# Kernel optimization log

Measured on AMD Instinct MI355X. Metric: run time of the kernel, lower is better.

Reference implementation:

```python
import jax, jax.numpy as jnp
import numpy as np

B_SZ, NX, IN_DIM = 32, 16384, 3
DIM, J, MODE, RANK, FC_DIM, OUT_DIM, N_LAYERS = 64, 16, 128, 4, 128, 1, 3


def setup_inputs() -> dict:
    key = jax.random.key(0)
    ks = jax.random.split(key, 20)
    scale = 1.0 / (MODE * MODE)
    s_out = 1.0 / MODE
    x = jax.random.normal(ks[0], (B_SZ, NX, IN_DIM), jnp.float32)
    bases = jax.random.normal(ks[1], (NX, MODE), jnp.float32) / np.sqrt(NX)
    wbases = jax.random.normal(ks[2], (NX, MODE), jnp.float32) / np.sqrt(NX)
    product = bases.T @ wbases  # (MODE_out, MODE_in)
    D_out = np.sqrt(s_out) * jax.random.uniform(ks[3], (J, MODE), jnp.float32)
    D_in = np.sqrt(s_out) * jax.random.uniform(ks[4], (J, MODE), jnp.float32)
    A = s_out * jax.random.uniform(ks[5], (J, RANK, MODE), jnp.float32)
    Bm = s_out * jax.random.uniform(ks[6], (J, RANK, MODE), jnp.float32)
    W_sp = scale * jax.random.normal(ks[7], (N_LAYERS, DIM, DIM, J), jnp.float32)
    W_conv = jax.random.normal(ks[8], (N_LAYERS, DIM, DIM), jnp.float32) / np.sqrt(DIM)
    b_conv = jnp.zeros((N_LAYERS, DIM), jnp.float32)
    W0 = jax.random.normal(ks[9], (IN_DIM, DIM), jnp.float32) / np.sqrt(IN_DIM)
    b0 = jnp.zeros((DIM,), jnp.float32)
    W1 = jax.random.normal(ks[10], (DIM, FC_DIM), jnp.float32) / np.sqrt(DIM)
    b1 = jnp.zeros((FC_DIM,), jnp.float32)
    W2 = jax.random.normal(ks[11], (FC_DIM, OUT_DIM), jnp.float32) / np.sqrt(FC_DIM)
    b2 = jnp.zeros((OUT_DIM,), jnp.float32)
    return {"x": x, "bases": bases, "wbases": wbases, "product": product,
            "D_out": D_out, "D_in": D_in, "A": A, "Bm": Bm,
            "W_sp": W_sp, "W_conv": W_conv, "b_conv": b_conv,
            "W0": W0, "b0": b0, "W1": W1, "b1": b1, "W2": W2, "b2": b2}


def reference(x, bases, wbases, product, D_out, D_in, A, Bm, W_sp, W_conv, b_conv,
              W0, b0, W1, b1, W2, b2):
    # fc0: (b, nx, in_dim) -> (b, nx, dim), then channel-first (b, dim, nx)
    h = jnp.swapaxes(x @ W0 + b0, 1, 2)
    # H construction: diag outer-products + low-rank A^T B update (mask_mode=0 so full add)
    H = D_out[:, :, None] * D_in[:, None, :] * product[None] \
        + jnp.einsum('jrk,jrl->jkl', A, Bm)  # (J, MODE, MODE)
    for i in range(N_LAYERS):
        xh = jnp.einsum('bcx,xk->bck', h, wbases)          # spectral transform
        xh1 = jnp.einsum('jkl,bil->bijk', H, xh)           # H mixing
        y = jnp.einsum('ioj,bijk->bok', W_sp[i], xh1)      # channel/kernel contraction
        x1 = jnp.einsum('bck,xk->bcx', y, bases)           # inverse transform
        x2 = jnp.einsum('oc,bcx->box', W_conv[i], h) + b_conv[i][None, :, None]
        h = x1 + x2
        if i != N_LAYERS - 1:
            h = jax.nn.gelu(h, approximate=False)
    h = jnp.swapaxes(h, 1, 2)  # (b, nx, dim)
    h = jax.nn.gelu(h @ W1 + b1, approximate=False)
    return h @ W2 + b2
```

## Files before the change

### kernel.cpp

```cpp
#include <hip/hip_runtime.h>
#include <hip/hip_bf16.h>
#include <math.h>

#define B_SZ   32
#define NXX    16384
#define IN_DIM 3
#define DIM    64
#define JM     16
#define MODE   128
#define RANKK  4
#define FC_DIM 128
#define N_LAY  3

typedef __attribute__((ext_vector_type(8))) short bf16x8;
typedef __attribute__((ext_vector_type(4))) float f32x4;
typedef unsigned short u16;

__device__ __forceinline__ float gelu_fast(float v) {
    float p = v * (0.7978845608f + 0.0356774081f * v * v);
    float e = __expf(-2.f * p);
    return v * __builtin_amdgcn_rcpf(1.f + e);
}
__device__ __forceinline__ u16 to_bf16(float v) {
    __hip_bfloat16 b = __float2bfloat16(v);
    return *(u16*)&b;
}

__global__ __launch_bounds__(256) void k_zero(float* __restrict__ p, int n) {
    int i = blockIdx.x * 256 + threadIdx.x;
    if (i < n) p[i] = 0.f;
}

__global__ __launch_bounds__(256) void k_build_H(
        const float* __restrict__ Dout, const float* __restrict__ Din,
        const float* __restrict__ product, const float* __restrict__ A,
        const float* __restrict__ Bm, u16* __restrict__ Hbf) {
    int idx = blockIdx.x * 256 + threadIdx.x;
    int j = idx >> 14;
    int k = (idx >> 7) & 127;
    int l = idx & 127;
    float v = Dout[j * MODE + k] * Din[j * MODE + l] * product[k * MODE + l];
#pragma unroll
    for (int r = 0; r < RANKK; ++r)
        v += A[(j * RANKK + r) * MODE + k] * Bm[(j * RANKK + r) * MODE + l];
    Hbf[idx] = to_bf16(v);
}

__global__ __launch_bounds__(256) void k_setup_wst(
        const float* __restrict__ Wsp, u16* __restrict__ WsT) {
    int idx = blockIdx.x * 256 + threadIdx.x;
    int i = idx & 63, o = (idx >> 6) & 63, j = (idx >> 12) & 15, lay = idx >> 16;
    WsT[idx] = to_bf16(Wsp[(((size_t)lay * 64 + i) * 64 + o) * 16 + j]);
}

__global__ __launch_bounds__(256) void k_setup_bases(
        const float* __restrict__ bases, u16* __restrict__ bh) {
    int idx = blockIdx.x * 256 + threadIdx.x;
    int x = idx >> 7, k = idx & 127;
    size_t off = (size_t)(k >> 3) * 131072 + (size_t)x * 8 + (k & 7);
    bh[off] = to_bf16(bases[idx]);
}

__global__ __launch_bounds__(256) void k_setup_wbT(
        const float* __restrict__ wb, u16* __restrict__ Th) {
    __shared__ float tile[32][33];
    int bx = blockIdx.x, bl = blockIdx.y;
    int t = threadIdx.x;
    int i = t >> 5, jj = t & 31;
#pragma unroll
    for (int r = 0; r < 4; ++r)
        tile[i + r * 8][jj] = wb[(size_t)(bx * 32 + i + r * 8) * MODE + bl * 32 + jj];
    __syncthreads();
#pragma unroll
    for (int r = 0; r < 4; ++r) {
        int l = bl * 32 + i + r * 8;
        int x = bx * 32 + jj;
        Th[(size_t)l * NXX + x] = to_bf16(tile[jj][i + r * 8]);
    }
}

__global__ __launch_bounds__(256) void k_setup_w1t(
        const float* __restrict__ W1, u16* __restrict__ wh) {
    int i = blockIdx.x * 256 + threadIdx.x;
    int f = i >> 6, c = i & 63;
    wh[i] = to_bf16(W1[c * FC_DIM + f]);
}

__global__ __launch_bounds__(256) void k_fc0(
        const float* __restrict__ x, const float* __restrict__ W0,
        const float* __restrict__ b0, u16* __restrict__ hh) {
    __shared__ float w0s[IN_DIM * DIM + DIM];
    int t = threadIdx.x;
    if (t < IN_DIM * DIM) w0s[t] = W0[t];
    if (t < DIM) w0s[IN_DIM * DIM + t] = b0[t];
    __syncthreads();
    int b = blockIdx.y;
    int xi = blockIdx.x * 32 + (t >> 3);
    int c8 = (t & 7) * 8;
    const float* xp = x + ((size_t)b * NXX + xi) * IN_DIM;
    float x0 = xp[0], x1 = xp[1], x2 = xp[2];
    u16 rh[8];
#pragma unroll
    for (int i = 0; i < 8; ++i) {
        int c = c8 + i;
        float v = x0 * w0s[c] + x1 * w0s[DIM + c] + x2 * w0s[2 * DIM + c]
                + w0s[3 * DIM + c];
        rh[i] = to_bf16(v);
    }
    size_t o = ((size_t)(b << 14) + xi) * 64 + c8;
    *(ushort4*)(hh + o)     = make_ushort4(rh[0], rh[1], rh[2], rh[3]);
    *(ushort4*)(hh + o + 4) = make_ushort4(rh[4], rh[5], rh[6], rh[7]);
}

#define SPAD 72
__global__ __launch_bounds__(256) void k_spectral_mfma(
        const u16* __restrict__ Hh,
        const u16* __restrict__ Wh,
        float* __restrict__ xh) {
    __shared__ u16 Ash[64 * SPAD];
    int t = threadIdx.x;
    int wave = t >> 6, lane = t & 63, quad = lane >> 4, l16 = lane & 15;
    int b = blockIdx.x;
    int x0 = blockIdx.y * 512;
    int cq = (t & 15) * 4;
    int xq = (t >> 4) * 4;
    int colw = (xq + ((t & 7) << 3)) & 63;
    const u16* srch = Hh + ((size_t)(b << 14) + x0 + xq) * 64 + cq;
    int l0 = wave * 32;
    const u16* w0h = Wh + (size_t)(l0 + l16) * NXX + x0;
    const u16* w1h = Wh + (size_t)(l0 + 16 + l16) * NXX + x0;
    f32x4 acc[4][2] = {};
    for (int kt = 0; kt < 512; kt += 64) {
        __syncthreads();
        {
            const u16* s = srch + (size_t)kt * 64;
            ushort4 r0 = *(const ushort4*)(s);
            ushort4 r1 = *(const ushort4*)(s + 64);
            ushort4 r2 = *(const ushort4*)(s + 128);
            ushort4 r3 = *(const ushort4*)(s + 192);
            *(ushort4*)&Ash[(cq + 0) * SPAD + colw] = make_ushort4(r0.x, r1.x, r2.x, r3.x);
            *(ushort4*)&Ash[(cq + 1) * SPAD + colw] = make_ushort4(r0.y, r1.y, r2.y, r3.y);
            *(ushort4*)&Ash[(cq + 2) * SPAD + colw] = make_ushort4(r0.z, r1.z, r2.z, r3.z);
            *(ushort4*)&Ash[(cq + 3) * SPAD + colw] = make_ushort4(r0.w, r1.w, r2.w, r3.w);
        }
        __syncthreads();
#pragma unroll
        for (int k0 = 0; k0 < 64; k0 += 32) {
            bf16x8 afh[4];
#pragma unroll
            for (int ct = 0; ct < 4; ++ct) {
                int rr = ct * 16 + l16;
                int ro = rr * SPAD + (((k0 + quad * 8) + (((rr >> 2) & 7) << 3)) & 63);
                afh[ct] = *(const bf16x8*)&Ash[ro];
            }
            int go = kt + k0 + quad * 8;
            bf16x8 b0h = *(const bf16x8*)(w0h + go);
            bf16x8 b1h = *(const bf16x8*)(w1h + go);
#pragma unroll
            for (int ct = 0; ct < 4; ++ct) {
                acc[ct][0] = __builtin_amdgcn_mfma_f32_16x16x32_bf16(afh[ct], b0h, acc[ct][0], 0, 0, 0);
                acc[ct][1] = __builtin_amdgcn_mfma_f32_16x16x32_bf16(afh[ct], b1h, acc[ct][1], 0, 0, 0);
            }
        }
    }
    float* xb = xh + (size_t)(b << 6) * 128;
#pragma unroll
    for (int ct = 0; ct < 4; ++ct)
#pragma unroll
        for (int lt = 0; lt < 2; ++lt)
#pragma unroll
            for (int r = 0; r < 4; ++r)
                atomicAdd(xb + (size_t)(ct * 16 + quad * 4 + r) * 128 + l0 + lt * 16 + l16,
                          acc[ct][lt][r]);
}

#define XPAD 136
#define TPAD 72
__global__ __launch_bounds__(256) void k_hmix_mfma(
        const float* __restrict__ xh, const u16* __restrict__ Hbf,
        const u16* __restrict__ WsT, float* __restrict__ y, int lay) {
    __shared__ u16 xsb[64 * XPAD];
    __shared__ u16 Ts[128 * TPAD];
    int t = threadIdx.x;
    int wave = t >> 6, lane = t & 63, quad = lane >> 4, l16 = lane & 15;
    int b = blockIdx.x, j = blockIdx.y;
    const float* xb = xh + (size_t)b * DIM * MODE;
    for (int idx = t; idx < DIM * MODE; idx += 256)
        xsb[(idx >> 7) * XPAD + (idx & 127)] = to_bf16(xb[idx]);
    __syncthreads();
    int k_base = wave * 32;
    {
        f32x4 acc[2][4] = {};
        const u16* Hj = Hbf + (size_t)j * MODE * MODE;
#pragma unroll
        for (int l0 = 0; l0 < 128; l0 += 32) {
            bf16x8 af[2], bf[4];
#pragma unroll
            for (int mt = 0; mt < 2; ++mt)
                af[mt] = *(const bf16x8*)(Hj + (size_t)(k_base + mt * 16 + l16) * 128 + l0 + quad * 8);
#pragma unroll
            for (int nt = 0; nt < 4; ++nt)
                bf[nt] = *(const bf16x8*)&xsb[(nt * 16 + l16) * XPAD + l0 + quad * 8];
#pragma unroll
            for (int mt = 0; mt < 2; ++mt)
#pragma unroll
                for (int nt = 0; nt < 4; ++nt)
                    acc[mt][nt] = __builtin_amdgcn_mfma_f32_16x16x32_bf16(af[mt], bf[nt], acc[mt][nt], 0, 0, 0);
        }
#pragma unroll
        for (int mt = 0; mt < 2; ++mt)
#pragma unroll
            for (int nt = 0; nt < 4; ++nt)
#pragma unroll
                for (int r = 0; r < 4; ++r)
                    Ts[(k_base + mt * 16 + quad * 4 + r) * TPAD + nt * 16 + l16] =
                        to_bf16(acc[mt][nt][r]);
    }
    __syncthreads();
    {
        f32x4 acc[4][2] = {};
        const u16* Wj = WsT + ((size_t)lay * JM + j) * DIM * DIM;
#pragma unroll
        for (int i0 = 0; i0 < 64; i0 += 32) {
            bf16x8 af[4], bf[2];
#pragma unroll
            for (int mt = 0; mt < 4; ++mt)
                af[mt] = *(const bf16x8*)(Wj + (size_t)(mt * 16 + l16) * 64 + i0 + quad * 8);
#pragma unroll
            for (int nt = 0; nt < 2; ++nt)
                bf[nt] = *(const bf16x8*)&Ts[(k_base + nt * 16 + l16) * TPAD + i0 + quad * 8];
#pragma unroll
            for (int mt = 0; mt < 4; ++mt)
#pragma unroll
                for (int nt = 0; nt < 2; ++nt)
                    acc[mt][nt] = __builtin_amdgcn_mfma_f32_16x16x32_bf16(af[mt], bf[nt], acc[mt][nt], 0, 0, 0);
        }
        float* yb = y + (size_t)b * DIM * MODE;
#pragma unroll
        for (int mt = 0; mt < 4; ++mt)
#pragma unroll
            for (int nt = 0; nt < 2; ++nt)
#pragma unroll
                for (int r = 0; r < 4; ++r)
                    atomicAdd(yb + (size_t)(mt * 16 + quad * 4 + r) * 128 + k_base + nt * 16 + l16,
                              acc[mt][nt][r]);
    }
}

__global__ __launch_bounds__(256) void k_build_A(
        const float* __restrict__ y, const float* __restrict__ Wconv,
        u16* __restrict__ Ah, int lay) {
    int b = blockIdx.x;
    for (int idx = threadIdx.x; idx < 12288; idx += 256) {
        int i = idx & 7, l16 = (idx >> 3) & 15, quad = (idx >> 7) & 3,
            ot = (idx >> 9) & 3, ks = idx >> 11;
        int o = ot * 16 + l16;
        int k = ks * 32 + quad * 8 + i;
        float v = (k < 128) ? y[((size_t)b * DIM + o) * MODE + k]
                            : Wconv[(size_t)lay * DIM * DIM + o * DIM + (k - 128)];
        Ah[(size_t)b * 12288 + idx] = to_bf16(v);
    }
}

#define CPAD 72
template <bool DO_MLP>
__global__ __launch_bounds__(256, 4) void k_inv_conv_mfma(
        const u16* __restrict__ Afh,
        const u16* __restrict__ Bfh,
        u16* __restrict__ Hh,
        const float* __restrict__ bconv, int lay,
        const u16* __restrict__ W1h,
        const float* __restrict__ b1, const float* __restrict__ W2,
        const float* __restrict__ b2, float* __restrict__ out) {
    __shared__ u16 hsh[128 * CPAD];
    int t = threadIdx.x;
    int wave = t >> 6, lane = t & 63, quad = lane >> 4, l16 = lane & 15;
    int b = blockIdx.x;
    int x0 = blockIdx.y * 128;
#pragma unroll
    for (int it = 0; it < 4; ++it) {
        int idx = it * 256 + t;
        int row = idx >> 3, c8 = (idx & 7) * 8;
        size_t src = ((size_t)(b << 14) + x0 + row) * 64 + c8;
        *(bf16x8*)&hsh[row * CPAD + c8] = *(const bf16x8*)(Hh + src);
    }
    __syncthreads();

    int xw = wave * 32;
    const u16* afb_h = Afh + (size_t)b * 12288;
    f32x4 acc[4][2] = {};
#pragma unroll
    for (int ks = 0; ks < 6; ++ks) {
        bf16x8 afh[4], bfh[2];
#pragma unroll
        for (int ot = 0; ot < 4; ++ot) {
            size_t ao = (size_t)(((ks * 4 + ot) * 4 + quad) * 16 + l16) * 8;
            afh[ot] = *(const bf16x8*)(afb_h + ao);
        }
#pragma unroll
        for (int x2 = 0; x2 < 2; ++x2) {
            int xl = xw + x2 * 16 + l16;
            if (ks < 4) {
                size_t bo = (size_t)((ks * 4 + quad) * 16384 + x0 + xl) * 8;
                bfh[x2] = *(const bf16x8*)(Bfh + bo);
            } else {
                int ko = (ks - 4) * 32 + quad * 8;
                bfh[x2] = *(const bf16x8*)&hsh[xl * CPAD + ko];
            }
        }
#pragma unroll
        for (int ot = 0; ot < 4; ++ot)
#pragma unroll
            for (int x2 = 0; x2 < 2; ++x2)
                acc[ot][x2] = __builtin_amdgcn_mfma_f32_16x16x32_bf16(afh[ot], bfh[x2], acc[ot][x2], 0, 0, 0);
    }
    __syncthreads();

#pragma unroll
    for (int ot = 0; ot < 4; ++ot) {
        float4 bc = *(const float4*)(bconv + lay * DIM + ot * 16 + quad * 4);
#pragma unroll
        for (int x2 = 0; x2 < 2; ++x2) {
            int xl = xw + x2 * 16 + l16;
            float vr[4] = {acc[ot][x2][0] + bc.x, acc[ot][x2][1] + bc.y,
                           acc[ot][x2][2] + bc.z, acc[ot][x2][3] + bc.w};
            if (!DO_MLP) {
#pragma unroll
                for (int r = 0; r < 4; ++r) vr[r] = gelu_fast(vr[r]);
            }
            ushort4 uh;
            uh.x = to_bf16(vr[0]); uh.y = to_bf16(vr[1]);
            uh.z = to_bf16(vr[2]); uh.w = to_bf16(vr[3]);
            *(ushort4*)&hsh[xl * CPAD + ot * 16 + quad * 4] = uh;
        }
    }
    __syncthreads();

    if (!DO_MLP) {
#pragma unroll
        for (int it = 0; it < 4; ++it) {
            int idx = it * 256 + t;
            int row = idx >> 3, c8 = (idx & 7) * 8;
            size_t dst = ((size_t)(b << 14) + x0 + row) * 64 + c8;
            *(bf16x8*)(Hh + dst) = *(const bf16x8*)&hsh[row * CPAD + c8];
        }
        return;
    }

#pragma unroll
    for (int x2 = 0; x2 < 2; ++x2) {
        bf16x8 ah[2];
#pragma unroll
        for (int ks = 0; ks < 2; ++ks) {
            int ro = (xw + x2 * 16 + l16) * CPAD + ks * 32 + quad * 8;
            ah[ks] = *(const bf16x8*)&hsh[ro];
        }
        float vo[4] = {0.f, 0.f, 0.f, 0.f};
#pragma unroll
        for (int ft = 0; ft < 8; ++ft) {
            f32x4 a2 = {};
#pragma unroll
            for (int ks = 0; ks < 2; ++ks) {
                size_t o = (size_t)(ft * 16 + l16) * 64 + ks * 32 + quad * 8;
                bf16x8 bh = *(const bf16x8*)(W1h + o);
                a2 = __builtin_amdgcn_mfma_f32_16x16x32_bf16(ah[ks], bh, a2, 0, 0, 0);
            }
            float bb = b1[ft * 16 + l16];
            float w2 = W2[ft * 16 + l16];
#pragma unroll
            for (int r = 0; r < 4; ++r)
                vo[r] += gelu_fast(a2[r] + bb) * w2;
        }
#pragma unroll
        for (int r = 0; r < 4; ++r) {
            float v = vo[r];
            v += __shfl_xor(v, 1);
            v += __shfl_xor(v, 2);
            v += __shfl_xor(v, 4);
            v += __shfl_xor(v, 8);
            vo[r] = v;
        }
        if (l16 == 0) {
            float bb2 = b2[0];
            float4 o4 = make_float4(vo[0] + bb2, vo[1] + bb2, vo[2] + bb2, vo[3] + bb2);
            *(float4*)(out + (size_t)b * NXX + x0 + xw + x2 * 16 + quad * 4) = o4;
        }
    }
}

extern "C" void kernel_launch(void* const* d_in, const int* in_sizes, int n_in,
                              void* d_out, int out_size, void* d_ws, size_t ws_size,
                              hipStream_t stream) {
    const float* x      = (const float*)d_in[0];
    const float* bases  = (const float*)d_in[1];
    const float* wbases = (const float*)d_in[2];
    const float* product= (const float*)d_in[3];
    const float* Dout   = (const float*)d_in[4];
    const float* Din    = (const float*)d_in[5];
    const float* A      = (const float*)d_in[6];
    const float* Bm     = (const float*)d_in[7];
    const float* Wsp    = (const float*)d_in[8];
    const float* Wconv  = (const float*)d_in[9];
    const float* bconv  = (const float*)d_in[10];
    const float* W0     = (const float*)d_in[11];
    const float* b0     = (const float*)d_in[12];
    const float* W1     = (const float*)d_in[13];
    const float* b1     = (const float*)d_in[14];
    const float* W2     = (const float*)d_in[15];
    const float* b2     = (const float*)d_in[16];
    float* out = (float*)d_out;

    const size_t need = 79314944;
    if (ws_size < need) {
        k_zero<<<dim3((out_size + 255) / 256), dim3(256), 0, stream>>>(out, out_size);
        return;
    }

    char* W = (char*)d_ws;
    size_t off = 0;
    auto alloc = [&](size_t bytes) { void* p = W + off; off += bytes; return p; };
    u16*   Hbf      = (u16*)alloc(524288);
    u16*   WsT      = (u16*)alloc(393216);
    u16*   bases_hi = (u16*)alloc(4194304);
    u16*   wbT_hi   = (u16*)alloc(4194304);
    u16*   Abuf_hi  = (u16*)alloc(786432);
    float* ybuf     = (float*)alloc(1048576);
    float* xh       = (float*)alloc(1048576);
    u16*   h_hi     = (u16*)alloc(67108864);
    u16*   w1t_hi   = (u16*)alloc(16384);

    k_build_H<<<dim3(1024), dim3(256), 0, stream>>>(Dout, Din, product, A, Bm, Hbf);
    k_setup_wst<<<dim3(768), dim3(256), 0, stream>>>(Wsp, WsT);
    k_setup_bases<<<dim3(8192), dim3(256), 0, stream>>>(bases, bases_hi);
    k_setup_wbT<<<dim3(512, 4), dim3(256), 0, stream>>>(wbases, wbT_hi);
    k_setup_w1t<<<dim3(32), dim3(256), 0, stream>>>(W1, w1t_hi);
    k_fc0<<<dim3(512, B_SZ), dim3(256), 0, stream>>>(x, W0, b0, h_hi);

    for (int lay = 0; lay < N_LAY; ++lay) {
        int last = (lay == N_LAY - 1);
        k_zero<<<dim3(2048), dim3(256), 0, stream>>>(ybuf, 524288);
        k_spectral_mfma<<<dim3(B_SZ, 32), dim3(256), 0, stream>>>(
            h_hi, wbT_hi, xh);
        k_hmix_mfma<<<dim3(B_SZ, JM), dim3(256), 0, stream>>>(
            xh, Hbf, WsT, ybuf, lay);
        k_build_A<<<dim3(B_SZ), dim3(256), 0, stream>>>(ybuf, Wconv, Abuf_hi, lay);
        dim3 g(B_SZ, 128), blk(256);
        if (last)
            k_inv_conv_mfma<true><<<g, blk, 0, stream>>>(
                Abuf_hi, bases_hi, h_hi, bconv, lay,
                w1t_hi, b1, W2, b2, out);
        else
            k_inv_conv_mfma<false><<<g, blk, 0, stream>>>(
                Abuf_hi, bases_hi, h_hi, bconv, lay,
                w1t_hi, b1, W2, b2, out);
    }
}
```

Measured before the change: 496.3 us.

## Double-buffer LDS tiles in spectral and inverse-conv kernels with register prefetch

The spectral kernel now prefetches the next 64-point h tile into registers while running MFMAs on the current LDS buffer, then writes it into the alternate buffer, removing one barrier per iteration. The inverse/conv kernel becomes persistent over four 128-point tiles (grid reduced 4x) and prefetches the next tile's h into registers while computing the current one, with double-buffered LDS. This is meant to hide global load latency behind compute, at the cost of doubled LDS use, more registers and fewer blocks, which may lower occupancy.

```diff
diff --git a/kernel.cpp b/kernel.cpp
--- a/kernel.cpp
+++ b/kernel.cpp
@@ -117,7 +117,7 @@
         const u16* __restrict__ Hh,
         const u16* __restrict__ Wh,
         float* __restrict__ xh) {
-    __shared__ u16 Ash[64 * SPAD];
+    __shared__ u16 Ash[2][64 * SPAD];
     int t = threadIdx.x;
     int wave = t >> 6, lane = t & 63, quad = lane >> 4, l16 = lane & 15;
     int b = blockIdx.x;
@@ -130,20 +130,29 @@
     const u16* w0h = Wh + (size_t)(l0 + l16) * NXX + x0;
     const u16* w1h = Wh + (size_t)(l0 + 16 + l16) * NXX + x0;
     f32x4 acc[4][2] = {};
-    for (int kt = 0; kt < 512; kt += 64) {
+    ushort4 r0, r1, r2, r3;
+    r0 = *(const ushort4*)(srch);
+    r1 = *(const ushort4*)(srch + 64);
+    r2 = *(const ushort4*)(srch + 128);
+    r3 = *(const ushort4*)(srch + 192);
+    {
+        u16* A = Ash[0];
+        *(ushort4*)&A[(cq + 0) * SPAD + colw] = make_ushort4(r0.x, r1.x, r2.x, r3.x);
+        *(ushort4*)&A[(cq + 1) * SPAD + colw] = make_ushort4(r0.y, r1.y, r2.y, r3.y);
+        *(ushort4*)&A[(cq + 2) * SPAD + colw] = make_ushort4(r0.z, r1.z, r2.z, r3.z);
+        *(ushort4*)&A[(cq + 3) * SPAD + colw] = make_ushort4(r0.w, r1.w, r2.w, r3.w);
+    }
+    for (int it = 0; it < 8; ++it) {
         __syncthreads();
-        {
-            const u16* s = srch + (size_t)kt * 64;
-            ushort4 r0 = *(const ushort4*)(s);
-            ushort4 r1 = *(const ushort4*)(s + 64);
-            ushort4 r2 = *(const ushort4*)(s + 128);
-            ushort4 r3 = *(const ushort4*)(s + 192);
-            *(ushort4*)&Ash[(cq + 0) * SPAD + colw] = make_ushort4(r0.x, r1.x, r2.x, r3.x);
-            *(ushort4*)&Ash[(cq + 1) * SPAD + colw] = make_ushort4(r0.y, r1.y, r2.y, r3.y);
-            *(ushort4*)&Ash[(cq + 2) * SPAD + colw] = make_ushort4(r0.z, r1.z, r2.z, r3.z);
-            *(ushort4*)&Ash[(cq + 3) * SPAD + colw] = make_ushort4(r0.w, r1.w, r2.w, r3.w);
-        }
-        __syncthreads();
+        int cur = it & 1;
+        if (it < 7) {
+            const u16* s = srch + (size_t)(it + 1) * 4096;
+            r0 = *(const ushort4*)(s);
+            r1 = *(const ushort4*)(s + 64);
+            r2 = *(const ushort4*)(s + 128);
+            r3 = *(const ushort4*)(s + 192);
+        }
+        const u16* A = Ash[cur];
 #pragma unroll
         for (int k0 = 0; k0 < 64; k0 += 32) {
             bf16x8 afh[4];
@@ -151,9 +160,9 @@
             for (int ct = 0; ct < 4; ++ct) {
                 int rr = ct * 16 + l16;
                 int ro = rr * SPAD + (((k0 + quad * 8) + (((rr >> 2) & 7) << 3)) & 63);
-                afh[ct] = *(const bf16x8*)&Ash[ro];
-            }
-            int go = kt + k0 + quad * 8;
+                afh[ct] = *(const bf16x8*)&A[ro];
+            }
+            int go = it * 64 + k0 + quad * 8;
             bf16x8 b0h = *(const bf16x8*)(w0h + go);
             bf16x8 b1h = *(const bf16x8*)(w1h + go);
 #pragma unroll
@@ -161,6 +170,13 @@
                 acc[ct][0] = __builtin_amdgcn_mfma_f32_16x16x32_bf16(afh[ct], b0h, acc[ct][0], 0, 0, 0);
                 acc[ct][1] = __builtin_amdgcn_mfma_f32_16x16x32_bf16(afh[ct], b1h, acc[ct][1], 0, 0, 0);
             }
+        }
+        if (it < 7) {
+            u16* An = Ash[1 - cur];
+            *(ushort4*)&An[(cq + 0) * SPAD + colw] = make_ushort4(r0.x, r1.x, r2.x, r3.x);
+            *(ushort4*)&An[(cq + 1) * SPAD + colw] = make_ushort4(r0.y, r1.y, r2.y, r3.y);
+            *(ushort4*)&An[(cq + 2) * SPAD + colw] = make_ushort4(r0.z, r1.z, r2.z, r3.z);
+            *(ushort4*)&An[(cq + 3) * SPAD + colw] = make_ushort4(r0.w, r1.w, r2.w, r3.w);
         }
     }
     float* xb = xh + (size_t)(b << 6) * 128;
@@ -272,118 +288,140 @@
         const u16* __restrict__ W1h,
         const float* __restrict__ b1, const float* __restrict__ W2,
         const float* __restrict__ b2, float* __restrict__ out) {
-    __shared__ u16 hsh[128 * CPAD];
+    __shared__ u16 hsh[2][128 * CPAD];
     int t = threadIdx.x;
     int wave = t >> 6, lane = t & 63, quad = lane >> 4, l16 = lane & 15;
     int b = blockIdx.x;
-    int x0 = blockIdx.y * 128;
-#pragma unroll
-    for (int it = 0; it < 4; ++it) {
-        int idx = it * 256 + t;
-        int row = idx >> 3, c8 = (idx & 7) * 8;
-        size_t src = ((size_t)(b << 14) + x0 + row) * 64 + c8;
-        *(bf16x8*)&hsh[row * CPAD + c8] = *(const bf16x8*)(Hh + src);
-    }
-    __syncthreads();
-
+    int xbase = blockIdx.y * 512;
     int xw = wave * 32;
     const u16* afb_h = Afh + (size_t)b * 12288;
-    f32x4 acc[4][2] = {};
-#pragma unroll
-    for (int ks = 0; ks < 6; ++ks) {
-        bf16x8 afh[4], bfh[2];
+    int srow = t >> 3, sc8 = (t & 7) * 8;
+
+    bf16x8 pf[4];
+#pragma unroll
+    for (int it = 0; it < 4; ++it) {
+        int row = srow + it * 32;
+        pf[it] = *(const bf16x8*)(Hh + ((size_t)(b << 14) + xbase + row) * 64 + sc8);
+    }
+#pragma unroll
+    for (int it = 0; it < 4; ++it)
+        *(bf16x8*)&hsh[0][(srow + it * 32) * CPAD + sc8] = pf[it];
+
+    for (int s = 0; s < 4; ++s) {
+        int cur = s & 1;
+        __syncthreads();
+        if (s < 3) {
+#pragma unroll
+            for (int it = 0; it < 4; ++it) {
+                int row = srow + it * 32;
+                pf[it] = *(const bf16x8*)(Hh + ((size_t)(b << 14) + xbase + (s + 1) * 128 + row) * 64 + sc8);
+            }
+        }
+        int x0 = xbase + s * 128;
+        const u16* hs = hsh[cur];
+        f32x4 acc[4][2] = {};
+#pragma unroll
+        for (int ks = 0; ks < 6; ++ks) {
+            bf16x8 afh[4], bfh[2];
+#pragma unroll
+            for (int ot = 0; ot < 4; ++ot) {
+                size_t ao = (size_t)(((ks * 4 + ot) * 4 + quad) * 16 + l16) * 8;
+                afh[ot] = *(const bf16x8*)(afb_h + ao);
+            }
+#pragma unroll
+            for (int x2 = 0; x2 < 2; ++x2) {
+                int xl = xw + x2 * 16 + l16;
+                if (ks < 4) {
+                    size_t bo = (size_t)((ks * 4 + quad) * 16384 + x0 + xl) * 8;
+                    bfh[x2] = *(const bf16x8*)(Bfh + bo);
+                } else {
+                    int ko = (ks - 4) * 32 + quad * 8;
+                    bfh[x2] = *(const bf16x8*)&hs[xl * CPAD + ko];
+                }
+            }
+#pragma unroll
+            for (int ot = 0; ot < 4; ++ot)
+#pragma unroll
+                for (int x2 = 0; x2 < 2; ++x2)
+                    acc[ot][x2] = __builtin_amdgcn_mfma_f32_16x16x32_bf16(afh[ot], bfh[x2], acc[ot][x2], 0, 0, 0);
+        }
+        __syncthreads();
+
+        u16* hw = hsh[cur];
 #pragma unroll
         for (int ot = 0; ot < 4; ++ot) {
-            size_t ao = (size_t)(((ks * 4 + ot) * 4 + quad) * 16 + l16) * 8;
-            afh[ot] = *(const bf16x8*)(afb_h + ao);
-        }
-#pragma unroll
-        for (int x2 = 0; x2 < 2; ++x2) {
-            int xl = xw + x2 * 16 + l16;
-            if (ks < 4) {
-                size_t bo = (size_t)((ks * 4 + quad) * 16384 + x0 + xl) * 8;
-                bfh[x2] = *(const bf16x8*)(Bfh + bo);
-            } else {
-                int ko = (ks - 4) * 32 + quad * 8;
-                bfh[x2] = *(const bf16x8*)&hsh[xl * CPAD + ko];
-            }
-        }
-#pragma unroll
-        for (int ot = 0; ot < 4; ++ot)
-#pragma unroll
-            for (int x2 = 0; x2 < 2; ++x2)
-                acc[ot][x2] = __builtin_amdgcn_mfma_f32_16x16x32_bf16(afh[ot], bfh[x2], acc[ot][x2], 0, 0, 0);
-    }
-    __syncthreads();
-
-#pragma unroll
-    for (int ot = 0; ot < 4; ++ot) {
-        float4 bc = *(const float4*)(bconv + lay * DIM + ot * 16 + quad * 4);
-#pragma unroll
-        for (int x2 = 0; x2 < 2; ++x2) {
-            int xl = xw + x2 * 16 + l16;
-            float vr[4] = {acc[ot][x2][0] + bc.x, acc[ot][x2][1] + bc.y,
-                           acc[ot][x2][2] + bc.z, acc[ot][x2][3] + bc.w};
-            if (!DO_MLP) {
-#pragma unroll
-                for (int r = 0; r < 4; ++r) vr[r] = gelu_fast(vr[r]);
-            }
-            ushort4 uh;
-            uh.x = to_bf16(vr[0]); uh.y = to_bf16(vr[1]);
-            uh.z = to_bf16(vr[2]); uh.w = to_bf16(vr[3]);
-            *(ushort4*)&hsh[xl * CPAD + ot * 16 + quad * 4] = uh;
-        }
-    }
-    __syncthreads();
-
-    if (!DO_MLP) {
-#pragma unroll
-        for (int it = 0; it < 4; ++it) {
-            int idx = it * 256 + t;
-            int row = idx >> 3, c8 = (idx & 7) * 8;
-            size_t dst = ((size_t)(b << 14) + x0 + row) * 64 + c8;
-            *(bf16x8*)(Hh + dst) = *(const bf16x8*)&hsh[row * CPAD + c8];
-        }
-        return;
-    }
-
-#pragma unroll
-    for (int x2 = 0; x2 < 2; ++x2) {
-        bf16x8 ah[2];
-#pragma unroll
-        for (int ks = 0; ks < 2; ++ks) {
-            int ro = (xw + x2 * 16 + l16) * CPAD + ks * 32 + quad * 8;
-            ah[ks] = *(const bf16x8*)&hsh[ro];
-        }
-        float vo[4] = {0.f, 0.f, 0.f, 0.f};
-#pragma unroll
-        for (int ft = 0; ft < 8; ++ft) {
-            f32x4 a2 = {};
-#pragma unroll
-            for (int ks = 0; ks < 2; ++ks) {
-                size_t o = (size_t)(ft * 16 + l16) * 64 + ks * 32 + quad * 8;
-                bf16x8 bh = *(const bf16x8*)(W1h + o);
-                a2 = __builtin_amdgcn_mfma_f32_16x16x32_bf16(ah[ks], bh, a2, 0, 0, 0);
-            }
-            float bb = b1[ft * 16 + l16];
-            float w2 = W2[ft * 16 + l16];
-#pragma unroll
-            for (int r = 0; r < 4; ++r)
-                vo[r] += gelu_fast(a2[r] + bb) * w2;
-        }
-#pragma unroll
-        for (int r = 0; r < 4; ++r) {
-            float v = vo[r];
-            v += __shfl_xor(v, 1);
-            v += __shfl_xor(v, 2);
-            v += __shfl_xor(v, 4);
-            v += __shfl_xor(v, 8);
-            vo[r] = v;
-        }
-        if (l16 == 0) {
-            float bb2 = b2[0];
-            float4 o4 = make_float4(vo[0] + bb2, vo[1] + bb2, vo[2] + bb2, vo[3] + bb2);
-            *(float4*)(out + (size_t)b * NXX + x0 + xw + x2 * 16 + quad * 4) = o4;
+            float4 bc = *(const float4*)(bconv + lay * DIM + ot * 16 + quad * 4);
+#pragma unroll
+            for (int x2 = 0; x2 < 2; ++x2) {
+                int xl = xw + x2 * 16 + l16;
+                float vr[4] = {acc[ot][x2][0] + bc.x, acc[ot][x2][1] + bc.y,
+                               acc[ot][x2][2] + bc.z, acc[ot][x2][3] + bc.w};
+                if (!DO_MLP) {
+#pragma unroll
+                    for (int r = 0; r < 4; ++r) vr[r] = gelu_fast(vr[r]);
+                }
+                ushort4 uh;
+                uh.x = to_bf16(vr[0]); uh.y = to_bf16(vr[1]);
+                uh.z = to_bf16(vr[2]); uh.w = to_bf16(vr[3]);
+                *(ushort4*)&hw[xl * CPAD + ot * 16 + quad * 4] = uh;
+            }
+        }
+
+        if (!DO_MLP) {
+            __syncthreads();
+#pragma unroll
+            for (int it = 0; it < 4; ++it) {
+                int row = srow + it * 32;
+                size_t dst = ((size_t)(b << 14) + x0 + row) * 64 + sc8;
+                *(bf16x8*)(Hh + dst) = *(const bf16x8*)&hw[row * CPAD + sc8];
+            }
+        } else {
+#pragma unroll
+            for (int x2 = 0; x2 < 2; ++x2) {
+                bf16x8 ah[2];
+#pragma unroll
+                for (int ks = 0; ks < 2; ++ks) {
+                    int ro = (xw + x2 * 16 + l16) * CPAD + ks * 32 + quad * 8;
+                    ah[ks] = *(const bf16x8*)&hw[ro];
+                }
+                float vo[4] = {0.f, 0.f, 0.f, 0.f};
+#pragma unroll
+                for (int ft = 0; ft < 8; ++ft) {
+                    f32x4 a2 = {};
+#pragma unroll
+                    for (int ks = 0; ks < 2; ++ks) {
+                        size_t o = (size_t)(ft * 16 + l16) * 64 + ks * 32 + quad * 8;
+                        bf16x8 bh = *(const bf16x8*)(W1h + o);
+                        a2 = __builtin_amdgcn_mfma_f32_16x16x32_bf16(ah[ks], bh, a2, 0, 0, 0);
+                    }
+                    float bb = b1[ft * 16 + l16];
+                    float w2 = W2[ft * 16 + l16];
+#pragma unroll
+                    for (int r = 0; r < 4; ++r)
+                        vo[r] += gelu_fast(a2[r] + bb) * w2;
+                }
+#pragma unroll
+                for (int r = 0; r < 4; ++r) {
+                    float v = vo[r];
+                    v += __shfl_xor(v, 1);
+                    v += __shfl_xor(v, 2);
+                    v += __shfl_xor(v, 4);
+                    v += __shfl_xor(v, 8);
+                    vo[r] = v;
+                }
+                if (l16 == 0) {
+                    float bb2 = b2[0];
+                    float4 o4 = make_float4(vo[0] + bb2, vo[1] + bb2, vo[2] + bb2, vo[3] + bb2);
+                    *(float4*)(out + (size_t)b * NXX + x0 + xw + x2 * 16 + quad * 4) = o4;
+                }
+            }
+        }
+
+        if (s < 3) {
+            u16* hn = hsh[1 - cur];
+#pragma unroll
+            for (int it = 0; it < 4; ++it)
+                *(bf16x8*)&hn[(srow + it * 32) * CPAD + sc8] = pf[it];
         }
     }
 }
@@ -444,7 +482,7 @@
         k_hmix_mfma<<<dim3(B_SZ, JM), dim3(256), 0, stream>>>(
             xh, Hbf, WsT, ybuf, lay);
         k_build_A<<<dim3(B_SZ), dim3(256), 0, stream>>>(ybuf, Wconv, Abuf_hi, lay);
-        dim3 g(B_SZ, 128), blk(256);
+        dim3 g(B_SZ, 32), blk(256);
         if (last)
             k_inv_conv_mfma<true><<<g, blk, 0, stream>>>(
                 Abuf_hi, bases_hi, h_hi, bconv, lay,
```

Result: slower. 695.3 us (+40.1%).
